# Optimization experiments

Measured on AMD Instinct MI355X. Metric: run time of the kernel, lower is better.

The kernel has to match this reference:

```python
import jax, jax.numpy as jnp
import numpy as np


def _cdist(p1, p2):
    # Euclidean cdist via the matmul expansion (matches torch.cdist p=2 fast path):
    # ||a-b||^2 = ||a||^2 + ||b||^2 - 2 a.b ; clamp tiny negatives before sqrt.
    sq1 = jnp.sum(p1 * p1, axis=-1, keepdims=True)        # (N, 1)
    sq2 = jnp.sum(p2 * p2, axis=-1, keepdims=True).T      # (1, M)
    d2 = sq1 + sq2 - 2.0 * (p1 @ p2.T)                    # (N, M)
    return jnp.sqrt(jnp.maximum(d2, 0.0))


def setup_inputs() -> dict:
    key = jax.random.key(0)
    k1, k2 = jax.random.split(key)
    N, M = 16384, 16384
    points1 = jax.random.normal(k1, (N, 3), dtype=jnp.float32)
    points2 = jax.random.normal(k2, (M, 3), dtype=jnp.float32)
    return {"points1": points1, "points2": points2}


def reference(points1, points2):
    dist = _cdist(points1, points2)                        # (N, M)
    min1 = jnp.min(dist, axis=1)                           # (N,) nearest in points2
    min2 = jnp.min(dist, axis=0)                           # (M,) nearest in points1
    return jnp.sum(min1) + jnp.sum(min2)
```

## Files before the change

### kernel.cpp

```cpp
#include <hip/hip_runtime.h>
#include <hip/hip_bf16.h>
#include <math.h>


typedef _Float16 half8    __attribute__((ext_vector_type(8)));
typedef float    floatx16 __attribute__((ext_vector_type(16)));

constexpr int CH    = 1024;
constexpr int RT    = 2;
constexpr int WROWS = RT * 32;
constexpr int ROWS  = 4 * WROWS;
constexpr int BLK   = 256;

__global__ __launch_bounds__(256) void init_kernel(unsigned* __restrict__ mins,
                                                   int n, float* __restrict__ out) {
    int i = blockIdx.x * blockDim.x + threadIdx.x;
    if (i < n) mins[i] = 0x7F800000u;
    if (i == 0) out[0] = 0.0f;
}

__global__ __launch_bounds__(BLK, 4) void chamfer_mfma_kernel(
    const float* __restrict__ P1, const float* __restrict__ P2,
    unsigned* __restrict__ min1, unsigned* __restrict__ min2,
    int n1, int n2)
{
    __shared__ uint2    sB[CH];
    __shared__ uint2    sZero;
    __shared__ unsigned sColMin[CH];
    __shared__ float    sRowMin[ROWS];

    const int tid  = threadIdx.x;
    const int wave = tid >> 6;
    const int lane = tid & 63;
    const int n    = lane & 31;
    const int g    = lane >> 5;
    const bool g0  = (g == 0);

    for (int i = tid; i < CH; i += BLK) sColMin[i] = 0x7F800000u;
    if (tid == 0) { sZero.x = 0u; sZero.y = 0u; }

    const int bstart = blockIdx.y * CH;
    for (int i = tid; i < CH; i += BLK) {
        int j = bstart + i; if (j >= n2) j = n2 - 1;
        float bx = P2[3*j], by = P2[3*j+1], bz = P2[3*j+2];
        _Float16 hx = (_Float16)bx, hy = (_Float16)by, hz = (_Float16)bz;
        float qx = (float)hx, qy = (float)hy, qz = (float)hz;
        _Float16 hw = (_Float16)(qx*qx + qy*qy + qz*qz);
        union { _Float16 h[4]; uint2 u; } p;
        p.h[0] = hx; p.h[1] = hy; p.h[2] = hz; p.h[3] = hw;
        sB[i] = p.u;
    }

    const _Float16 h0 = (_Float16)0.0f;
    half8 af[RT];
#pragma unroll
    for (int t = 0; t < RT; ++t) {
        int row = blockIdx.x * ROWS + wave * WROWS + t * 32 + n;
        if (row >= n1) row = n1 - 1;
        float ax = P1[3*row], ay = P1[3*row+1], az = P1[3*row+2];
        _Float16 hax = (_Float16)ax, hay = (_Float16)ay, haz = (_Float16)az;
        float qx = (float)hax, qy = (float)hay, qz = (float)haz;
        _Float16 hs = (_Float16)(qx*qx + qy*qy + qz*qz);
        af[t][0] = g0 ? (_Float16)(-2.0f * qx) : h0;
        af[t][1] = g0 ? (_Float16)(-2.0f * qy) : h0;
        af[t][2] = g0 ? (_Float16)(-2.0f * qz) : h0;
        af[t][3] = g0 ? (_Float16)1.0f : h0;
        af[t][4] = g0 ? hs : h0;
        af[t][5] = h0; af[t][6] = h0; af[t][7] = h0;
    }
    unsigned c2;
    { union { _Float16 h[2]; unsigned u; } q;
      q.h[0] = g0 ? (_Float16)1.0f : h0; q.h[1] = h0; c2 = q.u; }

    __syncthreads();

    floatx16 rowmin[RT];
#pragma unroll
    for (int t = 0; t < RT; ++t)
#pragma unroll
        for (int r = 0; r < 16; ++r) rowmin[t][r] = 1e30f;
    const floatx16 zacc = {};

    const uint2* bp   = g0 ? (sB + n) : (&sZero);
    const int    step = g0 ? 32 : 0;

#pragma unroll 2
    for (int bt = 0; bt < CH / 32; ++bt) {
        uint2 b = *bp; bp += step;
        union { half8 v; unsigned u[4]; } bu;
        bu.u[0] = b.x; bu.u[1] = b.y; bu.u[2] = c2; bu.u[3] = 0u;

        floatx16 d0 = __builtin_amdgcn_mfma_f32_32x32x16_f16(af[0], bu.v, zacc, 0, 0, 0);
        floatx16 d1 = __builtin_amdgcn_mfma_f32_32x32x16_f16(af[1], bu.v, zacc, 0, 0, 0);

#pragma unroll
        for (int r = 0; r < 16; ++r) {
            rowmin[0][r] = fminf(rowmin[0][r], d0[r]);
            rowmin[1][r] = fminf(rowmin[1][r], d1[r]);
        }

        float m[8];
#pragma unroll
        for (int r = 0; r < 8; ++r)
            m[r] = fminf(fminf(d0[2*r], d1[2*r]), fminf(d0[2*r+1], d1[2*r+1]));
        float c0 = fminf(fminf(m[0], m[1]), fminf(m[2], m[3]));
        float c1 = fminf(fminf(m[4], m[5]), fminf(m[6], m[7]));
        float cm = fmaxf(fminf(c0, c1), 0.0f);
        atomicMin(&sColMin[bt * 32 + n], __float_as_uint(cm));
    }

#pragma unroll
    for (int mask = 1; mask <= 16; mask <<= 1) {
#pragma unroll
        for (int t = 0; t < RT; ++t)
#pragma unroll
            for (int r = 0; r < 16; ++r)
                rowmin[t][r] = fminf(rowmin[t][r], __shfl_xor(rowmin[t][r], mask));
    }
    if (n == 0) {
#pragma unroll
        for (int t = 0; t < RT; ++t)
#pragma unroll
            for (int r = 0; r < 16; ++r) {
                int rr = wave * WROWS + t * 32 + g * 4 + ((r & 3) + 8 * (r >> 2));
                sRowMin[rr] = rowmin[t][r];
            }
    }
    __syncthreads();

    {
        int grow = blockIdx.x * ROWS + tid;
        if (grow < n1) {
            unsigned v = __float_as_uint(fmaxf(sRowMin[tid], 0.0f));
            unsigned cur = min1[grow];
            if (v < cur) atomicMin(&min1[grow], v);
        }
    }
    for (int i = tid; i < CH; i += BLK) {
        int j = bstart + i;
        if (j < n2) {
            unsigned v = sColMin[i];
            unsigned cur = min2[j];
            if (v < cur) atomicMin(&min2[j], v);
        }
    }
}

__global__ __launch_bounds__(256) void reduce_kernel(const unsigned* __restrict__ mins,
                                                     int ntot, float* __restrict__ out) {
    __shared__ float s[256];
    float acc = 0.0f;
    for (int i = blockIdx.x * 256 + threadIdx.x; i < ntot; i += gridDim.x * 256)
        acc += sqrtf(__uint_as_float(mins[i]));
    s[threadIdx.x] = acc;
    __syncthreads();
    for (int w = 128; w > 0; w >>= 1) {
        if (threadIdx.x < w) s[threadIdx.x] += s[threadIdx.x + w];
        __syncthreads();
    }
    if (threadIdx.x == 0) atomicAdd(out, s[0]);
}

extern "C" void kernel_launch(void* const* d_in, const int* in_sizes, int n_in,
                              void* d_out, int out_size, void* d_ws, size_t ws_size,
                              hipStream_t stream) {
    const float* P1 = (const float*)d_in[0];
    const float* P2 = (const float*)d_in[1];
    const int n1 = in_sizes[0] / 3;
    const int n2 = in_sizes[1] / 3;

    unsigned* min1 = (unsigned*)d_ws;
    unsigned* min2 = min1 + n1;
    float* out = (float*)d_out;

    {
        int n = n1 + n2;
        init_kernel<<<(n + 255) / 256, 256, 0, stream>>>(min1, n, out);
    }
    {
        dim3 grid((n1 + ROWS - 1) / ROWS, (n2 + CH - 1) / CH);
        chamfer_mfma_kernel<<<grid, BLK, 0, stream>>>(P1, P2, min1, min2, n1, n2);
    }
    reduce_kernel<<<64, 256, 0, stream>>>(min1, n1 + n2, out);
}
```

Measured before the change: 90.25 us.

## Replace column-min atomics with a symmetric two-direction row-min sweep

Instead of tracking column minima via shared-memory atomics and global atomicMin, the kernel is launched over both directions (P1→P2 and P2→P1) and each block only computes row minima, writing per-chunk partials. A two-stage reduction then takes min over chunks, sqrt, and sums deterministically. The column chunk size is doubled. This removes the per-tile column reduction and atomics but doubles the MFMA work and adds a partial-buffer round trip through global memory.

New measurement: 83.11 us. -7.9%, faster.

```diff
diff --git a/kernel.cpp b/kernel.cpp
--- a/kernel.cpp
+++ b/kernel.cpp
@@ -6,28 +6,25 @@
 typedef _Float16 half8    __attribute__((ext_vector_type(8)));
 typedef float    floatx16 __attribute__((ext_vector_type(16)));
 
-constexpr int CH    = 1024;
+constexpr int CH    = 2048;
 constexpr int RT    = 2;
 constexpr int WROWS = RT * 32;
 constexpr int ROWS  = 4 * WROWS;
 constexpr int BLK   = 256;
 
-__global__ __launch_bounds__(256) void init_kernel(unsigned* __restrict__ mins,
-                                                   int n, float* __restrict__ out) {
-    int i = blockIdx.x * blockDim.x + threadIdx.x;
-    if (i < n) mins[i] = 0x7F800000u;
-    if (i == 0) out[0] = 0.0f;
-}
+__global__ __launch_bounds__(BLK, 4) void chamfer_sweep_kernel(
+    const float* __restrict__ P1, const float* __restrict__ P2,
+    float* __restrict__ part, int n1, int n2, int YC)
+{
+    __shared__ uint2 sB[CH];
+    __shared__ float sRowMin[ROWS];
 
-__global__ __launch_bounds__(BLK, 4) void chamfer_mfma_kernel(
-    const float* __restrict__ P1, const float* __restrict__ P2,
-    unsigned* __restrict__ min1, unsigned* __restrict__ min2,
-    int n1, int n2)
-{
-    __shared__ uint2    sB[CH];
-    __shared__ uint2    sZero;
-    __shared__ unsigned sColMin[CH];
-    __shared__ float    sRowMin[ROWS];
+    const int dir  = blockIdx.z;
+    const float* A = dir == 0 ? P1 : P2;
+    const float* B = dir == 0 ? P2 : P1;
+    const int nA   = dir == 0 ? n1 : n2;
+    const int nB   = dir == 0 ? n2 : n1;
+    float* pbase   = part + (dir == 0 ? 0 : (size_t)YC * n1);
 
     const int tid  = threadIdx.x;
     const int wave = tid >> 6;
@@ -36,13 +33,10 @@
     const int g    = lane >> 5;
     const bool g0  = (g == 0);
 
-    for (int i = tid; i < CH; i += BLK) sColMin[i] = 0x7F800000u;
-    if (tid == 0) { sZero.x = 0u; sZero.y = 0u; }
-
     const int bstart = blockIdx.y * CH;
     for (int i = tid; i < CH; i += BLK) {
-        int j = bstart + i; if (j >= n2) j = n2 - 1;
-        float bx = P2[3*j], by = P2[3*j+1], bz = P2[3*j+2];
+        int j = bstart + i; if (j >= nB) j = nB - 1;
+        float bx = B[3*j], by = B[3*j+1], bz = B[3*j+2];
         _Float16 hx = (_Float16)bx, hy = (_Float16)by, hz = (_Float16)bz;
         float qx = (float)hx, qy = (float)hy, qz = (float)hz;
         _Float16 hw = (_Float16)(qx*qx + qy*qy + qz*qz);
@@ -56,8 +50,8 @@
 #pragma unroll
     for (int t = 0; t < RT; ++t) {
         int row = blockIdx.x * ROWS + wave * WROWS + t * 32 + n;
-        if (row >= n1) row = n1 - 1;
-        float ax = P1[3*row], ay = P1[3*row+1], az = P1[3*row+2];
+        if (row >= nA) row = nA - 1;
+        float ax = A[3*row], ay = A[3*row+1], az = A[3*row+2];
         _Float16 hax = (_Float16)ax, hay = (_Float16)ay, haz = (_Float16)az;
         float qx = (float)hax, qy = (float)hay, qz = (float)haz;
         _Float16 hs = (_Float16)(qx*qx + qy*qy + qz*qz);
@@ -70,7 +64,7 @@
     }
     unsigned c2;
     { union { _Float16 h[2]; unsigned u; } q;
-      q.h[0] = g0 ? (_Float16)1.0f : h0; q.h[1] = h0; c2 = q.u; }
+      q.h[0] = (_Float16)1.0f; q.h[1] = h0; c2 = q.u; }
 
     __syncthreads();
 
@@ -81,32 +75,24 @@
         for (int r = 0; r < 16; ++r) rowmin[t][r] = 1e30f;
     const floatx16 zacc = {};
 
-    const uint2* bp   = g0 ? (sB + n) : (&sZero);
-    const int    step = g0 ? 32 : 0;
+#pragma unroll 2
+    for (int bt = 0; bt < CH / 64; ++bt) {
+        uint2 b0 = sB[bt * 64 + n];
+        uint2 b1 = sB[bt * 64 + 32 + n];
+        union { half8 v; unsigned u[4]; } bu0, bu1;
+        bu0.u[0] = b0.x; bu0.u[1] = b0.y; bu0.u[2] = c2; bu0.u[3] = 0u;
+        bu1.u[0] = b1.x; bu1.u[1] = b1.y; bu1.u[2] = c2; bu1.u[3] = 0u;
 
-#pragma unroll 2
-    for (int bt = 0; bt < CH / 32; ++bt) {
-        uint2 b = *bp; bp += step;
-        union { half8 v; unsigned u[4]; } bu;
-        bu.u[0] = b.x; bu.u[1] = b.y; bu.u[2] = c2; bu.u[3] = 0u;
-
-        floatx16 d0 = __builtin_amdgcn_mfma_f32_32x32x16_f16(af[0], bu.v, zacc, 0, 0, 0);
-        floatx16 d1 = __builtin_amdgcn_mfma_f32_32x32x16_f16(af[1], bu.v, zacc, 0, 0, 0);
+        floatx16 d00 = __builtin_amdgcn_mfma_f32_32x32x16_f16(af[0], bu0.v, zacc, 0, 0, 0);
+        floatx16 d01 = __builtin_amdgcn_mfma_f32_32x32x16_f16(af[0], bu1.v, zacc, 0, 0, 0);
+        floatx16 d10 = __builtin_amdgcn_mfma_f32_32x32x16_f16(af[1], bu0.v, zacc, 0, 0, 0);
+        floatx16 d11 = __builtin_amdgcn_mfma_f32_32x32x16_f16(af[1], bu1.v, zacc, 0, 0, 0);
 
 #pragma unroll
         for (int r = 0; r < 16; ++r) {
-            rowmin[0][r] = fminf(rowmin[0][r], d0[r]);
-            rowmin[1][r] = fminf(rowmin[1][r], d1[r]);
+            rowmin[0][r] = fminf(fminf(rowmin[0][r], d00[r]), d01[r]);
+            rowmin[1][r] = fminf(fminf(rowmin[1][r], d10[r]), d11[r]);
         }
-
-        float m[8];
-#pragma unroll
-        for (int r = 0; r < 8; ++r)
-            m[r] = fminf(fminf(d0[2*r], d1[2*r]), fminf(d0[2*r+1], d1[2*r+1]));
-        float c0 = fminf(fminf(m[0], m[1]), fminf(m[2], m[3]));
-        float c1 = fminf(fminf(m[4], m[5]), fminf(m[6], m[7]));
-        float cm = fmaxf(fminf(c0, c1), 0.0f);
-        atomicMin(&sColMin[bt * 32 + n], __float_as_uint(cm));
     }
 
 #pragma unroll
@@ -130,35 +116,48 @@
 
     {
         int grow = blockIdx.x * ROWS + tid;
-        if (grow < n1) {
-            unsigned v = __float_as_uint(fmaxf(sRowMin[tid], 0.0f));
-            unsigned cur = min1[grow];
-            if (v < cur) atomicMin(&min1[grow], v);
-        }
-    }
-    for (int i = tid; i < CH; i += BLK) {
-        int j = bstart + i;
-        if (j < n2) {
-            unsigned v = sColMin[i];
-            unsigned cur = min2[j];
-            if (v < cur) atomicMin(&min2[j], v);
-        }
+        if (grow < nA) pbase[(size_t)blockIdx.y * nA + grow] = sRowMin[tid];
     }
 }
 
-__global__ __launch_bounds__(256) void reduce_kernel(const unsigned* __restrict__ mins,
-                                                     int ntot, float* __restrict__ out) {
+__global__ __launch_bounds__(256) void reduce1_kernel(
+    const float* __restrict__ part, float* __restrict__ bsum,
+    int n1, int n2, int YC)
+{
     __shared__ float s[256];
+    int r = blockIdx.x * 256 + threadIdx.x;
     float acc = 0.0f;
-    for (int i = blockIdx.x * 256 + threadIdx.x; i < ntot; i += gridDim.x * 256)
-        acc += sqrtf(__uint_as_float(mins[i]));
+    int ntot = n1 + n2;
+    if (r < ntot) {
+        const float* p; int row, nA;
+        if (r < n1) { p = part;                       row = r;      nA = n1; }
+        else        { p = part + (size_t)YC * n1;     row = r - n1; nA = n2; }
+        float m = 1e30f;
+        for (int y = 0; y < YC; ++y) m = fminf(m, p[(size_t)y * nA + row]);
+        acc = sqrtf(fmaxf(m, 0.0f));
+    }
     s[threadIdx.x] = acc;
     __syncthreads();
     for (int w = 128; w > 0; w >>= 1) {
         if (threadIdx.x < w) s[threadIdx.x] += s[threadIdx.x + w];
         __syncthreads();
     }
-    if (threadIdx.x == 0) atomicAdd(out, s[0]);
+    if (threadIdx.x == 0) bsum[blockIdx.x] = s[0];
+}
+
+__global__ __launch_bounds__(256) void reduce2_kernel(
+    const float* __restrict__ bsum, int nb, float* __restrict__ out)
+{
+    __shared__ float s[256];
+    float acc = 0.0f;
+    for (int i = threadIdx.x; i < nb; i += 256) acc += bsum[i];
+    s[threadIdx.x] = acc;
+    __syncthreads();
+    for (int w = 128; w > 0; w >>= 1) {
+        if (threadIdx.x < w) s[threadIdx.x] += s[threadIdx.x + w];
+        __syncthreads();
+    }
+    if (threadIdx.x == 0) out[0] = s[0];
 }
 
 extern "C" void kernel_launch(void* const* d_in, const int* in_sizes, int n_in,
@@ -168,18 +167,18 @@
     const float* P2 = (const float*)d_in[1];
     const int n1 = in_sizes[0] / 3;
     const int n2 = in_sizes[1] / 3;
+    const int nmax = (n1 > n2) ? n1 : n2;
+    const int YC = (nmax + CH - 1) / CH;
 
-    unsigned* min1 = (unsigned*)d_ws;
-    unsigned* min2 = min1 + n1;
-    float* out = (float*)d_out;
+    float* part = (float*)d_ws;
+    float* bsum = part + (size_t)YC * (n1 + n2);
+    float* out  = (float*)d_out;
 
     {
-        int n = n1 + n2;
-        init_kernel<<<(n + 255) / 256, 256, 0, stream>>>(min1, n, out);
+        dim3 grid((nmax + ROWS - 1) / ROWS, YC, 2);
+        chamfer_sweep_kernel<<<grid, BLK, 0, stream>>>(P1, P2, part, n1, n2, YC);
     }
-    {
-        dim3 grid((n1 + ROWS - 1) / ROWS, (n2 + CH - 1) / CH);
-        chamfer_mfma_kernel<<<grid, BLK, 0, stream>>>(P1, P2, min1, min2, n1, n2);
-    }
-    reduce_kernel<<<64, 256, 0, stream>>>(min1, n1 + n2, out);
+    int nb = (n1 + n2 + 255) / 256;
+    reduce1_kernel<<<nb, 256, 0, stream>>>(part, bsum, n1, n2, YC);
+    reduce2_kernel<<<1, 256, 0, stream>>>(bsum, nb, out);
 }
```
